# Optimization experiments

Hardware: AMD Instinct MI355X
Metric: run time of the kernel (lower is better)

The kernel has to match this reference:

```python
import jax, jax.numpy as jnp
import numpy as np

B, N, T, D, H, E = 2, 1024, 8, 128, 4, 8192
DH = D // H
NEG_SLOPE = 0.2  # GATv2Conv default negative_slope


def _ln(x, g, b):
    m = jnp.mean(x, -1, keepdims=True)
    v = jnp.mean((x - m) ** 2, -1, keepdims=True)
    return (x - m) * jax.lax.rsqrt(v + 1e-5) * g + b


def _forward(x, edge_index, gat_wl, gat_wr, gat_att, gat_b, in_w, in_b, out_w, out_b,
             ffn_w1, ffn_b1, ffn_w2, ffn_b2, fus_w, fus_b,
             lns_g, lns_b, lnt1_g, lnt1_b, lnt2_g, lnt2_b, lnf_g, lnf_b):
    # ---- spatial branch: GATv2, vectorized over (B, T) instead of python loops ----
    loops = jnp.arange(N)
    src = jnp.concatenate([edge_index[0], loops])  # j: message source (PyG adds self loops)
    dst = jnp.concatenate([edge_index[1], loops])  # i: aggregation target
    xl = jnp.einsum('bntd,de->bnte', x, gat_wl).reshape(B, N, T, H, D)
    xr = jnp.einsum('bntd,de->bnte', x, gat_wr).reshape(B, N, T, H, D)
    ml = xl[:, src]                                  # [B,Et,T,H,D]
    mr = xr[:, dst]
    e = jax.nn.leaky_relu(ml + mr, NEG_SLOPE)
    logits = jnp.einsum('bethd,hd->beth', e, gat_att)
    logits = jnp.moveaxis(logits, 1, 0)              # [Et,B,T,H]
    mx = jax.ops.segment_max(logits, dst, num_segments=N)
    p = jnp.exp(logits - mx[dst])                    # stable edge softmax per dst node
    ssum = jax.ops.segment_sum(p, dst, num_segments=N)
    alpha = p / ssum[dst]                            # [Et,B,T,H]
    msg = alpha[..., None] * jnp.moveaxis(ml, 1, 0)
    agg = jax.ops.segment_sum(msg, dst, num_segments=N)  # [N,B,T,H,D]
    x_sp = jnp.moveaxis(agg.mean(3), 0, 1) + gat_b   # concat=False -> head mean; [B,N,T,D]
    x_sp = _ln(x_sp, lns_g, lns_b)

    # ---- temporal branch: MHA + FFN, vectorized over all B*N nodes ----
    xt = x.reshape(B * N, T, D)
    qkv = xt @ in_w + in_b
    q, k, v = jnp.split(qkv, 3, axis=-1)
    q = q.reshape(B * N, T, H, DH)
    k = k.reshape(B * N, T, H, DH)
    v = v.reshape(B * N, T, H, DH)
    scores = jnp.einsum('bthd,bshd->bhts', q, k) / np.float32(np.sqrt(DH))
    attn = jax.nn.softmax(scores, -1)
    o = jnp.einsum('bhts,bshd->bthd', attn, v).reshape(B * N, T, D)
    o = o @ out_w + out_b
    x1 = _ln(xt + o, lnt1_g, lnt1_b)
    ffn = jax.nn.gelu(x1 @ ffn_w1 + ffn_b1, approximate=False) @ ffn_w2 + ffn_b2
    x_tp = _ln(x1 + ffn, lnt2_g, lnt2_b).reshape(B, N, T, D)

    # ---- gated fusion with residual ----
    g = jax.nn.sigmoid(jnp.concatenate([x_sp, x_tp], -1) @ fus_w + fus_b)
    return _ln(g * x_sp + (1.0 - g) * x_tp + x, lnf_g, lnf_b)


def setup_inputs() -> dict:
    key = jax.random.key(0)
    ks = jax.random.split(key, 12)
    s = 0.05
    f = jnp.float32
    return {
        'x': jax.random.normal(ks[0], (B, N, T, D), f),
        'edge_index': jax.random.randint(ks[1], (2, E), 0, N),
        'gat_wl': jax.random.normal(ks[2], (D, H * D), f) * s,
        'gat_wr': jax.random.normal(ks[3], (D, H * D), f) * s,
        'gat_att': jax.random.normal(ks[4], (H, D), f) * s,
        'gat_b': jnp.zeros((D,), f),
        'in_w': jax.random.normal(ks[5], (D, 3 * D), f) * s,
        'in_b': jnp.zeros((3 * D,), f),
        'out_w': jax.random.normal(ks[6], (D, D), f) * s,
        'out_b': jnp.zeros((D,), f),
        'ffn_w1': jax.random.normal(ks[7], (D, 4 * D), f) * s,
        'ffn_b1': jnp.zeros((4 * D,), f),
        'ffn_w2': jax.random.normal(ks[8], (4 * D, D), f) * s,
        'ffn_b2': jnp.zeros((D,), f),
        'fus_w': jax.random.normal(ks[9], (2 * D, D), f) * s,
        'fus_b': jnp.zeros((D,), f),
        'lns_g': jnp.ones((D,), f), 'lns_b': jnp.zeros((D,), f),
        'lnt1_g': jnp.ones((D,), f), 'lnt1_b': jnp.zeros((D,), f),
        'lnt2_g': jnp.ones((D,), f), 'lnt2_b': jnp.zeros((D,), f),
        'lnf_g': jnp.ones((D,), f), 'lnf_b': jnp.zeros((D,), f),
    }


def reference(x, edge_index, gat_wl, gat_wr, gat_att, gat_b, in_w, in_b, out_w, out_b,
              ffn_w1, ffn_b1, ffn_w2, ffn_b2, fus_w, fus_b,
              lns_g, lns_b, lnt1_g, lnt1_b, lnt2_g, lnt2_b, lnf_g, lnf_b):
    return _forward(x, edge_index, gat_wl, gat_wr, gat_att, gat_b, in_w, in_b, out_w, out_b,
                    ffn_w1, ffn_b1, ffn_w2, ffn_b2, fus_w, fus_b,
                    lns_g, lns_b, lnt1_g, lnt1_b, lnt2_g, lnt2_b, lnf_g, lnf_b)
```

## Files before the change

kernel.cpp:

```cpp
#include <hip/hip_runtime.h>
#include <math.h>

#define B_ 2
#define N_ 1024
#define T_ 8
#define D_ 128
#define H_ 4
#define E_ 8192
#define EN_ 9216
#define M_ 16384

typedef unsigned short u16;
using bf16x8 = __attribute__((ext_vector_type(8))) short;
using f32x4  = __attribute__((ext_vector_type(4))) float;

__device__ __forceinline__ float bf2f(unsigned int u) {
  return __uint_as_float(u << 16);
}
__device__ __forceinline__ u16 f2bf(float f) {
  unsigned int x = __float_as_uint(f);
  x += 0x7fffu + ((x >> 16) & 1u);
  return (u16)(x >> 16);
}
__device__ __forceinline__ void load8f(const u16* p, float* f) {
  uint4 u = *(const uint4*)p;
  f[0]=bf2f(u.x & 0xffffu); f[1]=bf2f(u.x >> 16);
  f[2]=bf2f(u.y & 0xffffu); f[3]=bf2f(u.y >> 16);
  f[4]=bf2f(u.z & 0xffffu); f[5]=bf2f(u.z >> 16);
  f[6]=bf2f(u.w & 0xffffu); f[7]=bf2f(u.w >> 16);
}
__device__ __forceinline__ void unpack8(uint4 u, float* f) {
  f[0]=bf2f(u.x & 0xffffu); f[1]=bf2f(u.x >> 16);
  f[2]=bf2f(u.y & 0xffffu); f[3]=bf2f(u.y >> 16);
  f[4]=bf2f(u.z & 0xffffu); f[5]=bf2f(u.z >> 16);
  f[6]=bf2f(u.w & 0xffffu); f[7]=bf2f(u.w >> 16);
}
__device__ __forceinline__ void gl2lds(const u16* g, u16* l) {
  __builtin_amdgcn_global_load_lds(
      (const __attribute__((address_space(1))) unsigned int*)(const void*)g,
      (__attribute__((address_space(3))) unsigned int*)(void*)l,
      16, 0, 0);
}

__device__ __forceinline__ size_t bt_row(int r) {
  return (size_t)(((r >> 13) << 3) | (r & 7)) * 1024 + ((r >> 3) & 1023);
}

__device__ __forceinline__ u16 conv_w_elem(int idx,
    const float* outw, const float* f1, const float* f2, const float* fw) {
  const float* src; int base, K, N;
  if      (idx < 196608) { src = outw; base = 180224; K = 128; N = 128; }
  else if (idx < 262144) { src = f1;   base = 196608; K = 128; N = 512; }
  else if (idx < 327680) { src = f2;   base = 262144; K = 512; N = 128; }
  else                   { src = fw;   base = 327680; K = 256; N = 128; }
  int o = idx - base;
  int n = o / K, k = o - n * K;
  return f2bf(src[k * N + n]);
}

__global__ __launch_bounds__(256) void proj_k(const float* __restrict__ x,
    const float* __restrict__ wl, const float* __restrict__ wr,
    const float* __restrict__ inw, const float* __restrict__ outw,
    const float* __restrict__ f1, const float* __restrict__ f2,
    const float* __restrict__ fw, const float* __restrict__ in_b,
    u16* __restrict__ XL, u16* __restrict__ XR, u16* __restrict__ QKV,
    u16* __restrict__ WBt,
    const int* __restrict__ ei, int* __restrict__ offs, int* __restrict__ srcs) {
  __shared__ u16 As[64 * 128];
  __shared__ u16 Bs[128 * 128];
  int bx = blockIdx.x, by = blockIdx.y;
  int tid = threadIdx.x;

  if (bx == 11) {
    int gid = by * 256 + tid;
    for (int idx = 180224 + gid; idx < 360448; idx += 65536)
      WBt[idx] = conv_w_elem(idx, outw, f1, f2, fw);
    if (by != 0) return;
    int* cnt  = (int*)As;
    int* curp = (int*)(As + 2048);
    int* wsum = (int*)Bs;
    for (int j = tid; j < N_; j += 256) cnt[j] = 0;
    __syncthreads();
    for (int e = tid; e < EN_; e += 256) {
      int d = (e < E_) ? ei[E_ + e] : (e - E_);
      atomicAdd(&cnt[d], 1);
    }
    __syncthreads();
    int b4 = tid * 4;
    int s0 = cnt[b4], s1 = cnt[b4 + 1], s2 = cnt[b4 + 2], s3 = cnt[b4 + 3];
    int tsum = s0 + s1 + s2 + s3;
    wsum[tid] = tsum;
    __syncthreads();
    for (int off = 1; off < 256; off <<= 1) {
      int v = (tid >= off) ? wsum[tid - off] : 0;
      __syncthreads();
      wsum[tid] += v;
      __syncthreads();
    }
    int excl = wsum[tid] - tsum;
    offs[b4] = excl;                curp[b4] = excl;
    offs[b4 + 1] = excl + s0;       curp[b4 + 1] = excl + s0;
    offs[b4 + 2] = excl + s0 + s1;  curp[b4 + 2] = excl + s0 + s1;
    offs[b4 + 3] = excl + s0 + s1 + s2;
    curp[b4 + 3] = excl + s0 + s1 + s2;
    if (tid == 255) offs[N_] = excl + tsum;
    __syncthreads();
    for (int e = tid; e < EN_; e += 256) {
      int d = (e < E_) ? ei[E_ + e] : (e - E_);
      int s = (e < E_) ? ei[e] : (e - E_);
      int pos = atomicAdd(&curp[d], 1);
      srcs[pos] = s;
    }
    return;
  }

  int lane = tid & 63, wid = tid >> 6;
  int lr = lane & 15, lk = lane >> 4;
  int wm = (wid >> 1) * 32, wn = (wid & 1) * 64;

  const float* wsrc; int NS, n0;
  if      (bx < 4) { wsrc = wl;  NS = 512; n0 = bx * 128; }
  else if (bx < 8) { wsrc = wr;  NS = 512; n0 = (bx - 4) * 128; }
  else             { wsrc = inw; NS = 384; n0 = (bx - 8) * 128; }

#pragma unroll
  for (int i = 0; i < 2; ++i) {
    int c = tid + i * 256;
    int row = c >> 3, seg = c & 7;
    int kc = seg >> 1, half = seg & 1;
    const float* xp = x + (size_t)(by * 64 + row) * 128 + kc * 32 + half * 16;
#pragma unroll
    for (int d = 0; d < 2; ++d) {
      float4 v0 = *(const float4*)(xp + d * 8);
      float4 v1 = *(const float4*)(xp + d * 8 + 4);
      u16 ob[8] = {f2bf(v0.x), f2bf(v0.y), f2bf(v0.z), f2bf(v0.w),
                   f2bf(v1.x), f2bf(v1.y), f2bf(v1.z), f2bf(v1.w)};
      int ch = (2 * half + d) ^ (row & 3);
      *(uint4*)&As[kc * 2048 + row * 32 + ch * 8] = *(uint4*)ob;
    }
  }
#pragma unroll
  for (int i = 0; i < 4; ++i) {
    int c = tid + i * 256;
    int nrow = c & 127, kseg = c >> 7;
    int kc = kseg >> 1, half = kseg & 1;
#pragma unroll
    for (int d = 0; d < 2; ++d) {
      int kb = kc * 32 + half * 16 + d * 8;
      u16 ob[8];
#pragma unroll
      for (int j = 0; j < 8; ++j)
        ob[j] = f2bf(wsrc[(size_t)(kb + j) * NS + n0 + nrow]);
      int ch = (2 * half + d) ^ (nrow & 3);
      *(uint4*)&Bs[kc * 4096 + nrow * 32 + ch * 8] = *(uint4*)ob;
    }
  }
  __syncthreads();

  f32x4 acc[2][4] = {};
#pragma unroll
  for (int kc = 0; kc < 4; ++kc) {
    bf16x8 bf[4];
#pragma unroll
    for (int ni = 0; ni < 4; ++ni) {
      int rb = wn + ni * 16 + lr;
      bf[ni] = *(const bf16x8*)&Bs[kc * 4096 + rb * 32 + (lk ^ (rb & 3)) * 8];
    }
#pragma unroll
    for (int mi = 0; mi < 2; ++mi) {
      int ra = wm + mi * 16 + lr;
      bf16x8 af = *(const bf16x8*)&As[kc * 2048 + ra * 32 + (lk ^ (ra & 3)) * 8];
#pragma unroll
      for (int ni = 0; ni < 4; ++ni)
        acc[mi][ni] = __builtin_amdgcn_mfma_f32_16x16x32_bf16(af, bf[ni], acc[mi][ni], 0, 0, 0);
    }
  }

  u16* Cb; int ldc_; int col0; const float* bias_; int remap;
  if (bx < 4)      { Cb = XL;  ldc_ = 512; col0 = bx * 128;       bias_ = nullptr; remap = 1; }
  else if (bx < 8) { Cb = XR;  ldc_ = 512; col0 = (bx - 4) * 128; bias_ = nullptr; remap = 1; }
  else             { Cb = QKV; ldc_ = 384; col0 = (bx - 8) * 128; bias_ = in_b;    remap = 0; }
  float bc[4];
#pragma unroll
  for (int ni = 0; ni < 4; ++ni)
    bc[ni] = bias_ ? bias_[col0 + wn + ni * 16 + lr] : 0.f;

  __syncthreads();
#pragma unroll
  for (int mi = 0; mi < 2; ++mi) {
#pragma unroll
    for (int r = 0; r < 4; ++r) {
      int rowl = wm + mi * 16 + lk * 4 + r;
#pragma unroll
      for (int ni = 0; ni < 4; ++ni) {
        int col = wn + ni * 16 + lr;
        As[rowl * 128 + (col ^ ((rowl & 7) << 3))] = f2bf(acc[mi][ni][r] + bc[ni]);
      }
    }
  }
  __syncthreads();
  {
    int chunk = tid & 15;
    int rbase = tid >> 4;
#pragma unroll
    for (int pass = 0; pass < 4; ++pass) {
      int rowl = pass * 16 + rbase;
      int row = by * 64 + rowl;
      size_t orow = remap ? bt_row(row) : (size_t)row;
      int sw = (chunk ^ (rowl & 7)) * 8;
      *(uint4*)&Cb[orow * ldc_ + col0 + chunk * 8] =
          *(const uint4*)&As[rowl * 128 + sw];
    }
  }
}

__global__ __launch_bounds__(256) void gat_k(const u16* __restrict__ XL,
    const u16* __restrict__ XR,
    const int* __restrict__ offs, const int* __restrict__ srcs,
    const float* __restrict__ att, const float* __restrict__ gb,
    const float* __restrict__ lng, const float* __restrict__ lnb,
    u16* __restrict__ XSP) {
  int bid = blockIdx.x;
  int lane = threadIdx.x & 63;
  int wid = threadIdx.x >> 6;
  int xcd = bid & 7;
  int slot = bid >> 3;
  int p = ((slot >> 8) << 3) | xcd;
  int n = (slot & 255) * 4 + wid;
  int b = p >> 3, t = p & 7;
  int dd = (lane & 15) * 8;
  size_t tokn = (size_t)(b * N_ + n) * 8 + t;
  const u16* XLs = XL + (size_t)p * 1024 * 512;

  float mr[8], av[8];
  load8f(XR + ((size_t)p * 1024 + n) * 512 + lane * 8, mr);
  *(float4*)&av[0] = *(const float4*)(att + lane * 8);
  *(float4*)&av[4] = *(const float4*)(att + lane * 8 + 4);

  int beg = offs[n], end = offs[n + 1];
  float sH = 0.f;
  float acc[8] = {0.f, 0.f, 0.f, 0.f, 0.f, 0.f, 0.f, 0.f};
  int i = beg;
  uint4 r0 = *(const uint4*)(XLs + (size_t)srcs[i] * 512 + lane * 8);
  uint4 r1 = r0;
  if (i + 1 < end)
    r1 = *(const uint4*)(XLs + (size_t)srcs[i + 1] * 512 + lane * 8);
  while (i + 1 < end) {
    uint4 c0 = r0, c1 = r1;
    if (i + 2 < end)
      r0 = *(const uint4*)(XLs + (size_t)srcs[i + 2] * 512 + lane * 8);
    if (i + 3 < end)
      r1 = *(const uint4*)(XLs + (size_t)srcs[i + 3] * 512 + lane * 8);
    float ml0[8], ml1[8];
    unpack8(c0, ml0);
    unpack8(c1, ml1);
    float d0 = 0.f, d1 = 0.f;
#pragma unroll
    for (int j = 0; j < 8; ++j) {
      float m0 = ml0[j] + mr[j];
      m0 = fmaxf(m0, 0.2f * m0);
      d0 += m0 * av[j];
      float m1 = ml1[j] + mr[j];
      m1 = fmaxf(m1, 0.2f * m1);
      d1 += m1 * av[j];
    }
    d0 += __shfl_xor(d0, 1, 64); d1 += __shfl_xor(d1, 1, 64);
    d0 += __shfl_xor(d0, 2, 64); d1 += __shfl_xor(d1, 2, 64);
    d0 += __shfl_xor(d0, 4, 64); d1 += __shfl_xor(d1, 4, 64);
    d0 += __shfl_xor(d0, 8, 64); d1 += __shfl_xor(d1, 8, 64);
    float p0 = __expf(d0), p1 = __expf(d1);
    sH += p0 + p1;
#pragma unroll
    for (int j = 0; j < 8; ++j) acc[j] += p0 * ml0[j] + p1 * ml1[j];
    i += 2;
  }
  if (i < end) {
    float ml0[8];
    unpack8(r0, ml0);
    float d0 = 0.f;
#pragma unroll
    for (int j = 0; j < 8; ++j) {
      float m0 = ml0[j] + mr[j];
      m0 = fmaxf(m0, 0.2f * m0);
      d0 += m0 * av[j];
    }
    d0 += __shfl_xor(d0, 1, 64);
    d0 += __shfl_xor(d0, 2, 64);
    d0 += __shfl_xor(d0, 4, 64);
    d0 += __shfl_xor(d0, 8, 64);
    float p0 = __expf(d0);
    sH += p0;
#pragma unroll
    for (int j = 0; j < 8; ++j) acc[j] += p0 * ml0[j];
  }
  float invS = 1.f / sH;
#pragma unroll
  for (int j = 0; j < 8; ++j) acc[j] *= invS;
#pragma unroll
  for (int j = 0; j < 8; ++j) {
    acc[j] += __shfl_xor(acc[j], 16, 64);
    acc[j] += __shfl_xor(acc[j], 32, 64);
  }
#pragma unroll
  for (int j = 0; j < 8; ++j) acc[j] = acc[j] * 0.25f + gb[dd + j];
  float s = 0.f, s2 = 0.f;
#pragma unroll
  for (int j = 0; j < 8; ++j) { s += acc[j]; s2 += acc[j] * acc[j]; }
#pragma unroll
  for (int m = 1; m < 16; m <<= 1) {
    s += __shfl_xor(s, m, 64);
    s2 += __shfl_xor(s2, m, 64);
  }
  float mean = s * (1.f / 128.f);
  float var = s2 * (1.f / 128.f) - mean * mean;
  float r = rsqrtf(var + 1e-5f);
  if (lane < 16) {
    u16 ob[8];
#pragma unroll
    for (int j = 0; j < 8; ++j)
      ob[j] = f2bf((acc[j] - mean) * r * lng[dd + j] + lnb[dd + j]);
    *(uint4*)&XSP[tokn * 128 + dd] = *(uint4*)ob;
  }
}

__global__ __launch_bounds__(256) void tower_k(const u16* __restrict__ QKV,
    const u16* __restrict__ WTO, const float* __restrict__ out_b,
    const float* __restrict__ x,
    const float* __restrict__ lnt1_g, const float* __restrict__ lnt1_b,
    const u16* __restrict__ WTF1, const u16* __restrict__ WTF2,
    const float* __restrict__ b1, const float* __restrict__ b2,
    const float* __restrict__ lnt2_g, const float* __restrict__ lnt2_b,
    const u16* __restrict__ WTFUS, const float* __restrict__ fus_b,
    const float* __restrict__ lnf_g, const float* __restrict__ lnf_b,
    const u16* __restrict__ XSP, float* __restrict__ o32) {
  __shared__ u16 P[32 * 128];
  __shared__ u16 Wb[16384];
  __shared__ u16 Hc[4096];
  __shared__ float rs[64], rq[64];
  int by = blockIdx.x;
  int tid = threadIdx.x;
  int lane = tid & 63, wid = tid >> 6;
  int lr = lane & 15, lk = lane >> 4;
  int wm = (wid >> 1) * 16, wn = (wid & 1) * 64;

#pragma unroll
  for (int i = 0; i < 8; ++i) {
    int o = tid * 16 + i * 4096;
    int c = o >> 13;
    int wb = o & 8191;
    int nrow = wb >> 6;
    int kin = (wb & 63) >> 1;
    gl2lds(WTO + (size_t)nrow * 128 + c * 32 + kin,
           (u16*)((char*)Wb + wid * 1024 + i * 4096));
  }
  int t = lane >> 3, sidx = lane & 7, dg = lane & 7;
  for (int it = 0; it < 4; ++it) {
    int task = wid * 4 + it;
    int bnl = task >> 2, h = task & 3;
    int bn = by * 4 + bnl;
    const u16* base = QKV + (size_t)bn * 8 * 384;
    float va[8][4];
#pragma unroll
    for (int s2 = 0; s2 < 8; ++s2) {
      ushort4 vv = *(const ushort4*)(base + s2 * 384 + 256 + h * 32 + dg * 4);
      va[s2][0] = bf2f(vv.x); va[s2][1] = bf2f(vv.y);
      va[s2][2] = bf2f(vv.z); va[s2][3] = bf2f(vv.w);
    }
    const u16* qp = base + t * 384 + h * 32;
    const u16* kp = base + sidx * 384 + 128 + h * 32;
    float sc = 0.f;
#pragma unroll
    for (int d0 = 0; d0 < 32; d0 += 8) {
      float q[8], k[8];
      load8f(qp + d0, q);
      load8f(kp + d0, k);
#pragma unroll
      for (int j = 0; j < 8; ++j) sc += q[j] * k[j];
    }
    sc *= 0.17677669529663687f;
    float m = sc;
    m = fmaxf(m, __shfl_xor(m, 1, 64));
    m = fmaxf(m, __shfl_xor(m, 2, 64));
    m = fmaxf(m, __shfl_xor(m, 4, 64));
    float p = __expf(sc - m);
    float S = p;
    S += __shfl_xor(S, 1, 64);
    S += __shfl_xor(S, 2, 64);
    S += __shfl_xor(S, 4, 64);
    float alpha = p / S;
    int tb = lane & 56;
    float o0 = 0.f, o1 = 0.f, o2 = 0.f, o3 = 0.f;
#pragma unroll
    for (int s2 = 0; s2 < 8; ++s2) {
      float a = __shfl(alpha, tb + s2, 64);
      o0 += a * va[s2][0];
      o1 += a * va[s2][1];
      o2 += a * va[s2][2];
      o3 += a * va[s2][3];
    }
    u16 ov[4] = {f2bf(o0), f2bf(o1), f2bf(o2), f2bf(o3)};
    int row = bnl * 8 + t;
    *(ushort4*)&P[h * 1024 + row * 32 + dg * 4] = *(ushort4*)ov;
  }
  __syncthreads();

  f32x4 acc[4] = {};
#pragma unroll
  for (int c = 0; c < 4; ++c) {
    bf16x8 bf[4];
#pragma unroll
    for (int ni = 0; ni < 4; ++ni)
      bf[ni] = *(const bf16x8*)&Wb[c * 4096 + (wn + ni * 16 + lr) * 32 + lk * 8];
    bf16x8 af = *(const bf16x8*)&P[c * 1024 + (wm + lr) * 32 + lk * 8];
#pragma unroll
    for (int ni = 0; ni < 4; ++ni)
      acc[ni] = __builtin_amdgcn_mfma_f32_16x16x32_bf16(af, bf[ni], acc[ni], 0, 0, 0);
  }

  f32x4 x1r[4];
  {
    float bc[4];
#pragma unroll
    for (int ni = 0; ni < 4; ++ni) bc[ni] = out_b[wn + ni * 16 + lr];
#pragma unroll
    for (int r = 0; r < 4; ++r) {
      int rowl = wm + lk * 4 + r;
      int row = by * 32 + rowl;
      float s = 0.f, s2 = 0.f;
#pragma unroll
      for (int ni = 0; ni < 4; ++ni) {
        int col = wn + ni * 16 + lr;
        float v = acc[ni][r] + bc[ni] + x[(size_t)row * 128 + col];
        acc[ni][r] = v;
        s += v; s2 += v * v;
      }
      s += __shfl_xor(s, 1, 64); s2 += __shfl_xor(s2, 1, 64);
      s += __shfl_xor(s, 2, 64); s2 += __shfl_xor(s2, 2, 64);
      s += __shfl_xor(s, 4, 64); s2 += __shfl_xor(s2, 4, 64);
      s += __shfl_xor(s, 8, 64); s2 += __shfl_xor(s2, 8, 64);
      if (lr == 0) {
        rs[rowl * 2 + (wid & 1)] = s;
        rq[rowl * 2 + (wid & 1)] = s2;
      }
    }
    __syncthreads();
#pragma unroll
    for (int r = 0; r < 4; ++r) {
      int rowl = wm + lk * 4 + r;
      float tot = rs[rowl * 2] + rs[rowl * 2 + 1];
      float tq = rq[rowl * 2] + rq[rowl * 2 + 1];
      float mean = tot * (1.f / 128.f);
      float var = tq * (1.f / 128.f) - mean * mean;
      float rinv = rsqrtf(var + 1e-5f);
#pragma unroll
      for (int ni = 0; ni < 4; ++ni) {
        int col = wn + ni * 16 + lr;
        float o = (acc[ni][r] - mean) * rinv * lnt1_g[col] + lnt1_b[col];
        x1r[ni][r] = o;
        P[(col >> 5) * 1024 + rowl * 32 + (col & 31)] = f2bf(o);
      }
    }
  }

  int wr0 = (wid >> 1) * 16, wc0 = (wid & 1) * 32;
  f32x4 acc2[4] = {};
  for (int nc = 0; nc < 8; ++nc) {
    __syncthreads();
#pragma unroll
    for (int kc = 0; kc < 4; ++kc) {
      gl2lds(WTF1 + (size_t)(nc * 64 + (tid >> 2)) * 128 + kc * 32 + (tid & 3) * 8,
             (u16*)((char*)Wb + kc * 4096 + wid * 1024));
    }
#pragma unroll
    for (int i = 0; i < 4; ++i) {
      int o = tid * 16 + i * 4096;
      int kc2l = o >> 13;
      int wb = o & 8191;
      int nrow = wb >> 6;
      int kin = (wb & 63) >> 1;
      gl2lds(WTF2 + (size_t)nrow * 512 + nc * 64 + kc2l * 32 + kin,
             (u16*)((char*)Wb + 16384 + wid * 1024 + i * 4096));
    }
    __syncthreads();
    f32x4 a1[2] = {};
#pragma unroll
    for (int kc = 0; kc < 4; ++kc) {
      bf16x8 bf0 = *(const bf16x8*)&Wb[kc * 2048 + (wc0 + lr) * 32 + lk * 8];
      bf16x8 bf1 = *(const bf16x8*)&Wb[kc * 2048 + (wc0 + 16 + lr) * 32 + lk * 8];
      bf16x8 af = *(const bf16x8*)&P[kc * 1024 + (wr0 + lr) * 32 + lk * 8];
      a1[0] = __builtin_amdgcn_mfma_f32_16x16x32_bf16(af, bf0, a1[0], 0, 0, 0);
      a1[1] = __builtin_amdgcn_mfma_f32_16x16x32_bf16(af, bf1, a1[1], 0, 0, 0);
    }
#pragma unroll
    for (int r = 0; r < 4; ++r) {
      int row = wr0 + lk * 4 + r;
#pragma unroll
      for (int ni = 0; ni < 2; ++ni) {
        int cl = wc0 + ni * 16 + lr;
        float v = a1[ni][r] + b1[nc * 64 + cl];
        v = 0.5f * v * (1.f + erff(v * 0.70710678118f));
        Hc[(cl >> 5) * 1280 + row * 40 + (cl & 31)] = f2bf(v);
      }
    }
    __syncthreads();
#pragma unroll
    for (int kc2l = 0; kc2l < 2; ++kc2l) {
      bf16x8 bf[4];
#pragma unroll
      for (int ni = 0; ni < 4; ++ni)
        bf[ni] = *(const bf16x8*)&Wb[8192 + kc2l * 4096 + (wn + ni * 16 + lr) * 32 + lk * 8];
      bf16x8 af = *(const bf16x8*)&Hc[kc2l * 1280 + (wm + lr) * 40 + lk * 8];
#pragma unroll
      for (int ni = 0; ni < 4; ++ni)
        acc2[ni] = __builtin_amdgcn_mfma_f32_16x16x32_bf16(af, bf[ni], acc2[ni], 0, 0, 0);
    }
  }
  __syncthreads();

#pragma unroll
  for (int i = 0; i < 8; ++i) {
    int o = tid * 16 + i * 4096;
    int rl = o >> 6;
    int kcf = rl >> 7;
    int nrow = rl & 127;
    int kin = (o & 63) >> 1;
    gl2lds(WTFUS + (size_t)nrow * 256 + kcf * 32 + kin,
           (u16*)((char*)Wb + wid * 1024 + i * 4096));
  }
#pragma unroll
  for (int i = 0; i < 2; ++i) {
    int o = tid * 16 + i * 4096;
    int rl = o >> 6;
    int kcf = rl >> 5;
    int rowl = rl & 31;
    int kin = (o & 63) >> 1;
    gl2lds(XSP + (size_t)(by * 32 + rowl) * 128 + kcf * 32 + kin,
           (u16*)((char*)Hc + wid * 1024 + i * 4096));
  }

  {
    float bc[4];
#pragma unroll
    for (int ni = 0; ni < 4; ++ni) bc[ni] = b2[wn + ni * 16 + lr];
#pragma unroll
    for (int r = 0; r < 4; ++r) {
      int rowl = wm + lk * 4 + r;
      float s = 0.f, s2 = 0.f;
#pragma unroll
      for (int ni = 0; ni < 4; ++ni) {
        float v = acc2[ni][r] + bc[ni] + x1r[ni][r];
        acc2[ni][r] = v;
        s += v; s2 += v * v;
      }
      s += __shfl_xor(s, 1, 64); s2 += __shfl_xor(s2, 1, 64);
      s += __shfl_xor(s, 2, 64); s2 += __shfl_xor(s2, 2, 64);
      s += __shfl_xor(s, 4, 64); s2 += __shfl_xor(s2, 4, 64);
      s += __shfl_xor(s, 8, 64); s2 += __shfl_xor(s2, 8, 64);
      if (lr == 0) {
        rs[rowl * 2 + (wid & 1)] = s;
        rq[rowl * 2 + (wid & 1)] = s2;
      }
    }
    __syncthreads();
#pragma unroll
    for (int r = 0; r < 4; ++r) {
      int rowl = wm + lk * 4 + r;
      float tot = rs[rowl * 2] + rs[rowl * 2 + 1];
      float tq = rq[rowl * 2] + rq[rowl * 2 + 1];
      float mean = tot * (1.f / 128.f);
      float var = tq * (1.f / 128.f) - mean * mean;
      float rinv = rsqrtf(var + 1e-5f);
#pragma unroll
      for (int ni = 0; ni < 4; ++ni) {
        int col = wn + ni * 16 + lr;
        float o = (acc2[ni][r] - mean) * rinv * lnt2_g[col] + lnt2_b[col];
        acc2[ni][r] = o;
        P[rowl * 128 + (col ^ ((rowl & 7) << 3))] = f2bf(o);
      }
    }
  }
  __syncthreads();

  f32x4 acc3[4] = {};
#pragma unroll
  for (int kc = 0; kc < 4; ++kc) {
    bf16x8 bf[4];
#pragma unroll
    for (int ni = 0; ni < 4; ++ni)
      bf[ni] = *(const bf16x8*)&Wb[kc * 4096 + (wn + ni * 16 + lr) * 32 + lk * 8];
    bf16x8 af = *(const bf16x8*)&Hc[kc * 1024 + (wm + lr) * 32 + lk * 8];
#pragma unroll
    for (int ni = 0; ni < 4; ++ni)
      acc3[ni] = __builtin_amdgcn_mfma_f32_16x16x32_bf16(af, bf[ni], acc3[ni], 0, 0, 0);
  }
  __syncthreads();
#pragma unroll
  for (int i = 0; i < 8; ++i) {
    int o = tid * 16 + i * 4096;
    int rl = o >> 6;
    int kcf = rl >> 7;
    int nrow = rl & 127;
    int kin = (o & 63) >> 1;
    gl2lds(WTFUS + (size_t)nrow * 256 + 128 + kcf * 32 + kin,
           (u16*)((char*)Wb + wid * 1024 + i * 4096));
  }
  __syncthreads();
#pragma unroll
  for (int kc = 0; kc < 4; ++kc) {
    bf16x8 bf[4];
#pragma unroll
    for (int ni = 0; ni < 4; ++ni)
      bf[ni] = *(const bf16x8*)&Wb[kc * 4096 + (wn + ni * 16 + lr) * 32 + lk * 8];
    int arow = wm + lr;
    bf16x8 af = *(const bf16x8*)&P[arow * 128 + ((kc * 32 + lk * 8) ^ ((arow & 7) << 3))];
#pragma unroll
    for (int ni = 0; ni < 4; ++ni)
      acc3[ni] = __builtin_amdgcn_mfma_f32_16x16x32_bf16(af, bf[ni], acc3[ni], 0, 0, 0);
  }
  {
    float bc[4];
#pragma unroll
    for (int ni = 0; ni < 4; ++ni) bc[ni] = fus_b[wn + ni * 16 + lr];
#pragma unroll
    for (int r = 0; r < 4; ++r) {
      int rowl = wm + lk * 4 + r;
      int row = by * 32 + rowl;
      float s = 0.f, s2 = 0.f;
#pragma unroll
      for (int ni = 0; ni < 4; ++ni) {
        int col = wn + ni * 16 + lr;
        float v = acc3[ni][r] + bc[ni];
        float gg = 1.f / (1.f + __expf(-v));
        float xsp = bf2f((unsigned int)Hc[(col >> 5) * 1024 + rowl * 32 + (col & 31)]);
        float xtp = acc2[ni][r];
        v = gg * xsp + (1.f - gg) * xtp + x[(size_t)row * 128 + col];
        acc3[ni][r] = v;
        s += v; s2 += v * v;
      }
      s += __shfl_xor(s, 1, 64); s2 += __shfl_xor(s2, 1, 64);
      s += __shfl_xor(s, 2, 64); s2 += __shfl_xor(s2, 2, 64);
      s += __shfl_xor(s, 4, 64); s2 += __shfl_xor(s2, 4, 64);
      s += __shfl_xor(s, 8, 64); s2 += __shfl_xor(s2, 8, 64);
      if (lr == 0) {
        rs[rowl * 2 + (wid & 1)] = s;
        rq[rowl * 2 + (wid & 1)] = s2;
      }
    }
    __syncthreads();
#pragma unroll
    for (int r = 0; r < 4; ++r) {
      int rowl = wm + lk * 4 + r;
      int row = by * 32 + rowl;
      float tot = rs[rowl * 2] + rs[rowl * 2 + 1];
      float tq = rq[rowl * 2] + rq[rowl * 2 + 1];
      float mean = tot * (1.f / 128.f);
      float var = tq * (1.f / 128.f) - mean * mean;
      float rinv = rsqrtf(var + 1e-5f);
#pragma unroll
      for (int ni = 0; ni < 4; ++ni) {
        int col = wn + ni * 16 + lr;
        o32[(size_t)row * 128 + col] =
            (acc3[ni][r] - mean) * rinv * lnf_g[col] + lnf_b[col];
      }
    }
  }
}

extern "C" void kernel_launch(void* const* d_in, const int* in_sizes, int n_in,
                              void* d_out, int out_size, void* d_ws, size_t ws_size,
                              hipStream_t stream) {
  const float* x       = (const float*)d_in[0];
  const int*   ei      = (const int*)d_in[1];
  const float* gat_att = (const float*)d_in[4];
  const float* gat_b   = (const float*)d_in[5];
  const float* in_b    = (const float*)d_in[7];
  const float* out_b   = (const float*)d_in[9];
  const float* ffn_b1  = (const float*)d_in[11];
  const float* ffn_b2  = (const float*)d_in[13];
  const float* fus_b   = (const float*)d_in[15];
  const float* lns_g   = (const float*)d_in[16];
  const float* lns_b   = (const float*)d_in[17];
  const float* lnt1_g  = (const float*)d_in[18];
  const float* lnt1_b  = (const float*)d_in[19];
  const float* lnt2_g  = (const float*)d_in[20];
  const float* lnt2_b  = (const float*)d_in[21];
  const float* lnf_g   = (const float*)d_in[22];
  const float* lnf_b   = (const float*)d_in[23];

  char* ws = (char*)d_ws;
  u16*   WB    = (u16*)ws;
  u16*   WTO   = WB + 180224;
  u16*   WTF1  = WB + 196608;
  u16*   WTF2  = WB + 262144;
  u16*   WTFUS = WB + 327680;
  int*   OFFS  = (int*)(ws + 3145728);
  int*   SRCS  = (int*)(ws + 3153920);
  u16*   XL   = (u16*)(ws + 8388608);
  u16*   XR   = (u16*)(ws + 25165824);
  u16*   QKV  = (u16*)(ws + 50331648);
  u16*   XSP  = (u16*)(ws + 67108864);

  proj_k<<<dim3(12, 256), dim3(256), 0, stream>>>(x,
      (const float*)d_in[2], (const float*)d_in[3], (const float*)d_in[6],
      (const float*)d_in[8], (const float*)d_in[10], (const float*)d_in[12],
      (const float*)d_in[14], in_b, XL, XR, QKV, WB, ei, OFFS, SRCS);

  gat_k<<<dim3(4096), dim3(256), 0, stream>>>(XL, XR, OFFS, SRCS,
      gat_att, gat_b, lns_g, lns_b, XSP);

  tower_k<<<dim3(512), dim3(256), 0, stream>>>(QKV, WTO, out_b, x,
      lnt1_g, lnt1_b, WTF1, WTF2, ffn_b1, ffn_b2, lnt2_g, lnt2_b,
      WTFUS, fus_b, lnf_g, lnf_b, XSP, (float*)d_out);
}
```

Measured before the change: 196.4 us.

## Load A operand directly into registers and store GEMM output straight to global

The projection GEMM no longer stages the x tile in shared memory. Each lane loads its MFMA A-fragment straight from global memory into registers and converts it to bf16 there. The epilogue also drops the shared-memory transpose and writes each bf16 result element directly to global memory. This cuts LDS use and removes two barriers, but it replaces 16-byte coalesced output stores with scattered 2-byte stores and adds register pressure.

```diff
diff --git a/kernel.cpp b/kernel.cpp
--- a/kernel.cpp
+++ b/kernel.cpp
@@ -66,7 +66,6 @@
     u16* __restrict__ XL, u16* __restrict__ XR, u16* __restrict__ QKV,
     u16* __restrict__ WBt,
     const int* __restrict__ ei, int* __restrict__ offs, int* __restrict__ srcs) {
-  __shared__ u16 As[64 * 128];
   __shared__ u16 Bs[128 * 128];
   int bx = blockIdx.x, by = blockIdx.y;
   int tid = threadIdx.x;
@@ -76,9 +75,9 @@
     for (int idx = 180224 + gid; idx < 360448; idx += 65536)
       WBt[idx] = conv_w_elem(idx, outw, f1, f2, fw);
     if (by != 0) return;
-    int* cnt  = (int*)As;
-    int* curp = (int*)(As + 2048);
-    int* wsum = (int*)Bs;
+    int* cnt  = (int*)Bs;
+    int* curp = (int*)(Bs + 2048);
+    int* wsum = (int*)(Bs + 4096);
     for (int j = tid; j < N_; j += 256) cnt[j] = 0;
     __syncthreads();
     for (int e = tid; e < EN_; e += 256) {
@@ -123,22 +122,18 @@
   else if (bx < 8) { wsrc = wr;  NS = 512; n0 = (bx - 4) * 128; }
   else             { wsrc = inw; NS = 384; n0 = (bx - 8) * 128; }
 
-#pragma unroll
-  for (int i = 0; i < 2; ++i) {
-    int c = tid + i * 256;
-    int row = c >> 3, seg = c & 7;
-    int kc = seg >> 1, half = seg & 1;
-    const float* xp = x + (size_t)(by * 64 + row) * 128 + kc * 32 + half * 16;
-#pragma unroll
-    for (int d = 0; d < 2; ++d) {
-      float4 v0 = *(const float4*)(xp + d * 8);
-      float4 v1 = *(const float4*)(xp + d * 8 + 4);
-      u16 ob[8] = {f2bf(v0.x), f2bf(v0.y), f2bf(v0.z), f2bf(v0.w),
-                   f2bf(v1.x), f2bf(v1.y), f2bf(v1.z), f2bf(v1.w)};
-      int ch = (2 * half + d) ^ (row & 3);
-      *(uint4*)&As[kc * 2048 + row * 32 + ch * 8] = *(uint4*)ob;
-    }
-  }
+  float4 ar[4][2][2];
+  const float* xb = x + (size_t)(by * 64) * 128;
+#pragma unroll
+  for (int kc = 0; kc < 4; ++kc) {
+#pragma unroll
+    for (int mi = 0; mi < 2; ++mi) {
+      const float* p = xb + (size_t)(wm + mi * 16 + lr) * 128 + kc * 32 + lk * 8;
+      ar[kc][mi][0] = *(const float4*)p;
+      ar[kc][mi][1] = *(const float4*)(p + 4);
+    }
+  }
+
 #pragma unroll
   for (int i = 0; i < 4; ++i) {
     int c = tid + i * 256;
@@ -155,6 +150,18 @@
       *(uint4*)&Bs[kc * 4096 + nrow * 32 + ch * 8] = *(uint4*)ob;
     }
   }
+
+  bf16x8 afr[4][2];
+#pragma unroll
+  for (int kc = 0; kc < 4; ++kc) {
+#pragma unroll
+    for (int mi = 0; mi < 2; ++mi) {
+      float4 v0 = ar[kc][mi][0], v1 = ar[kc][mi][1];
+      u16 ob[8] = {f2bf(v0.x), f2bf(v0.y), f2bf(v0.z), f2bf(v0.w),
+                   f2bf(v1.x), f2bf(v1.y), f2bf(v1.z), f2bf(v1.w)};
+      afr[kc][mi] = *(const bf16x8*)ob;
+    }
+  }
   __syncthreads();
 
   f32x4 acc[2][4] = {};
@@ -168,11 +175,9 @@
     }
 #pragma unroll
     for (int mi = 0; mi < 2; ++mi) {
-      int ra = wm + mi * 16 + lr;
-      bf16x8 af = *(const bf16x8*)&As[kc * 2048 + ra * 32 + (lk ^ (ra & 3)) * 8];
 #pragma unroll
       for (int ni = 0; ni < 4; ++ni)
-        acc[mi][ni] = __builtin_amdgcn_mfma_f32_16x16x32_bf16(af, bf[ni], acc[mi][ni], 0, 0, 0);
+        acc[mi][ni] = __builtin_amdgcn_mfma_f32_16x16x32_bf16(afr[kc][mi], bf[ni], acc[mi][ni], 0, 0, 0);
     }
   }
 
@@ -185,31 +190,17 @@
   for (int ni = 0; ni < 4; ++ni)
     bc[ni] = bias_ ? bias_[col0 + wn + ni * 16 + lr] : 0.f;
 
-  __syncthreads();
 #pragma unroll
   for (int mi = 0; mi < 2; ++mi) {
 #pragma unroll
     for (int r = 0; r < 4; ++r) {
-      int rowl = wm + mi * 16 + lk * 4 + r;
+      int row = by * 64 + wm + mi * 16 + lk * 4 + r;
+      size_t orow = remap ? bt_row(row) : (size_t)row;
 #pragma unroll
       for (int ni = 0; ni < 4; ++ni) {
-        int col = wn + ni * 16 + lr;
-        As[rowl * 128 + (col ^ ((rowl & 7) << 3))] = f2bf(acc[mi][ni][r] + bc[ni]);
-      }
-    }
-  }
-  __syncthreads();
-  {
-    int chunk = tid & 15;
-    int rbase = tid >> 4;
-#pragma unroll
-    for (int pass = 0; pass < 4; ++pass) {
-      int rowl = pass * 16 + rbase;
-      int row = by * 64 + rowl;
-      size_t orow = remap ? bt_row(row) : (size_t)row;
-      int sw = (chunk ^ (rowl & 7)) * 8;
-      *(uint4*)&Cb[orow * ldc_ + col0 + chunk * 8] =
-          *(const uint4*)&As[rowl * 128 + sw];
+        int col = col0 + wn + ni * 16 + lr;
+        Cb[orow * ldc_ + col] = f2bf(acc[mi][ni][r] + bc[ni]);
+      }
     }
   }
 }
```

New measurement: 204.0 us. 1.04x slower.
